# Performance work log

Hardware: AMD Instinct MI355X
Metric: run time of the kernel (lower is better)

## Reference

```python
import jax, jax.numpy as jnp
import numpy as np

N = 100000      # nodes
E = 800000      # edges (before self-loops)
G = 128         # graphs
IN = 64         # per-table embedding dim (6 tables -> 384 input features)
L = 128         # layer_embd
OUT = 128       # out_embd
H = 2           # attention heads (concat=False -> mean over heads)
VOCABS = [33, 5, 3, 4, 2, 3]
NEG_SLOPE = 0.2
BN_EPS = 1e-5


def _seg_softmax(logits, seg, n):
    # softmax of per-edge/per-node logits grouped by segment id
    m = jax.ops.segment_max(logits, seg, num_segments=n)
    e = jnp.exp(logits - m[seg])
    s = jax.ops.segment_sum(e, seg, num_segments=n)
    return e / (s[seg] + 1e-16)


def _gat_conv(x, W, a_src, a_dst, b, src, dst, n):
    # PyG GATConv, add_self_loops already applied to (src,dst), concat=False
    h = (x @ W).reshape(n, H, -1)                 # [N,H,C]
    al_s = jnp.sum(h * a_src, axis=-1)            # [N,H]
    al_d = jnp.sum(h * a_dst, axis=-1)            # [N,H]
    e = jax.nn.leaky_relu(al_s[src] + al_d[dst], NEG_SLOPE)   # [E,H]
    alpha = _seg_softmax(e, dst, n)               # softmax over each dst's in-edges
    msg = h[src] * alpha[:, :, None]              # [E,H,C]
    out = jax.ops.segment_sum(msg, dst, num_segments=n)       # [N,H,C]
    return out.mean(axis=1) + b                   # head-mean + bias


def setup_inputs() -> dict:
    key = jax.random.key(0)
    ks = jax.random.split(key, 40)
    cols = [jax.random.randint(ks[i], (N, 1), 0, VOCABS[i]) for i in range(6)]
    x = jnp.concatenate(cols, axis=1).astype(jnp.int64)
    edge_index = jax.random.randint(ks[6], (2, E), 0, N).astype(jnp.int64)
    edge_type = jax.random.randint(ks[7], (E,), 0, 4).astype(jnp.int64)
    batch = jnp.sort(jax.random.randint(ks[8], (N,), 0, G)).astype(jnp.int64)
    s = 0.05
    p = {}
    for i in range(6):
        p[f"emb{i}"] = jax.random.normal(ks[10 + i], (VOCABS[i], IN)) * s
    p["W1"] = jax.random.normal(ks[16], (6 * IN, H * L)) * s
    p["as1"] = jax.random.normal(ks[17], (H, L)) * s
    p["ad1"] = jax.random.normal(ks[18], (H, L)) * s
    p["b1"] = jnp.zeros((L,))
    p["W2"] = jax.random.normal(ks[19], (L, H * OUT)) * s
    p["as2"] = jax.random.normal(ks[20], (H, OUT)) * s
    p["ad2"] = jax.random.normal(ks[21], (H, OUT)) * s
    p["b2"] = jnp.zeros((OUT,))
    p["gw1"] = jax.random.normal(ks[22], (OUT, OUT)) * s
    p["gb1"] = jnp.zeros((OUT,))
    p["bn_g"] = jnp.ones((OUT,))
    p["bn_b"] = jnp.zeros((OUT,))
    p["bn_m"] = jnp.zeros((OUT,))
    p["bn_v"] = jnp.ones((OUT,))
    p["gw2"] = jax.random.normal(ks[23], (OUT, 1)) * s
    p["gb2"] = jnp.zeros((1,))
    p["glw"] = jax.random.normal(ks[24], (OUT, 1)) * s
    p["glb"] = jnp.zeros((1,))
    return dict(x=x, edge_index=edge_index, edge_type=edge_type, batch=batch, **p)


def reference(x, edge_index, edge_type, batch,
              emb0, emb1, emb2, emb3, emb4, emb5,
              W1, as1, ad1, b1, W2, as2, ad2, b2,
              gw1, gb1, bn_g, bn_b, bn_m, bn_v, gw2, gb2, glw, glb):
    n = x.shape[0]
    embs = [emb0, emb1, emb2, emb3, emb4, emb5]
    x_ = jnp.concatenate([embs[i][x[:, i]] for i in range(6)], axis=1)  # [N, 6*IN]
    loops = jnp.arange(n)
    src = jnp.concatenate([edge_index[0], loops])
    dst = jnp.concatenate([edge_index[1], loops])
    out = jax.nn.sigmoid(_gat_conv(x_, W1, as1, ad1, b1, src, dst, n))
    out = jax.nn.sigmoid(_gat_conv(out, W2, as2, ad2, b2, src, dst, n))
    # GlobalAttention pooling (eval-mode BatchNorm in gate_nn)
    gh = out @ gw1 + gb1
    gh = (gh - bn_m) / jnp.sqrt(bn_v + BN_EPS) * bn_g + bn_b
    gh = jax.nn.relu(gh)
    logits = gh @ gw2 + gb2                       # [N,1]
    gate = _seg_softmax(logits, batch, G)         # softmax over nodes per graph
    pooled = jax.ops.segment_sum(gate * out, batch, num_segments=G)  # [G,OUT]
    return jax.nn.sigmoid(pooled @ glw + glb)     # [G,1]
```

## Files before the change

kernel.cpp:

```cpp
#include <hip/hip_runtime.h>
#include <hip/hip_bf16.h>
#include <hip/hip_fp16.h>

#define NN 100000
#define EE 800000
#define GG 128

typedef short bf16x8 __attribute__((ext_vector_type(8)));
typedef float f32x4 __attribute__((ext_vector_type(4)));
typedef float f32x2 __attribute__((ext_vector_type(2)));

__device__ __forceinline__ float bf2f(unsigned short v) {
    union { unsigned int u; float f; } x; x.u = ((unsigned int)v) << 16; return x.f;
}
__device__ __forceinline__ unsigned short f2bf(float f) {
    union { float f; unsigned int u; } x; x.f = f;
    unsigned int r = x.u + 0x7fffu + ((x.u >> 16) & 1u);
    return (unsigned short)(r >> 16);
}
__device__ __forceinline__ float sigmoidf_(float x) { return 1.f / (1.f + __expf(-x)); }
__device__ __forceinline__ float ldp(const void* p, int i, int f) {
    return f ? ((const float*)p)[i] : bf2f(((const unsigned short*)p)[i]);
}

#if defined(__has_builtin)
#if __has_builtin(__builtin_amdgcn_cvt_pk_f32_fp8) && __has_builtin(__builtin_amdgcn_cvt_pk_fp8_f32)
#define USE_HW_FP8 1
#endif
#endif
#ifndef USE_HW_FP8
#define USE_HW_FP8 0
#endif

#if USE_HW_FP8
__device__ __forceinline__ int fp8_pack2(float a, float b) {
    return __builtin_amdgcn_cvt_pk_fp8_f32(a, b, 0, false);
}
__device__ __forceinline__ void fp8_dec4v(unsigned int q, f32x2& lo, f32x2& hi) {
    lo = __builtin_amdgcn_cvt_pk_f32_fp8((int)q, false);
    hi = __builtin_amdgcn_cvt_pk_f32_fp8((int)q, true);
}
#else
__device__ __forceinline__ unsigned char f2bf8(float f) {
    unsigned short u = __half_as_ushort(__float2half(f));
    unsigned short r = u + 0x7f + ((u >> 8) & 1);
    return (unsigned char)(r >> 8);
}
__device__ __forceinline__ int fp8_pack2(float a, float b) {
    return (int)f2bf8(a) | ((int)f2bf8(b) << 8);
}
__device__ __forceinline__ float bf8_dec(unsigned int b) {
    return __half2float(__ushort_as_half((unsigned short)(b << 8)));
}
__device__ __forceinline__ void fp8_dec4v(unsigned int q, f32x2& lo, f32x2& hi) {
    lo[0] = bf8_dec(q & 0xff); lo[1] = bf8_dec((q >> 8) & 0xff);
    hi[0] = bf8_dec((q >> 16) & 0xff); hi[1] = bf8_dec(q >> 24);
}
#endif

__global__ void k_probe2(const unsigned int* __restrict__ w, const int* __restrict__ ei,
                         int* __restrict__ fflag, int* __restrict__ iflag) {
    __shared__ int s[256];
    int t = threadIdx.x;
    if (blockIdx.x == 0) {
        int cnt = 0;
        for (int i = t; i < 1024; i += 256) {
            unsigned int v = w[i];
            int e = (v >> 7) & 0xff;
            cnt += (e >= 100 && e <= 127) ? 1 : 0;
        }
        s[t] = cnt; __syncthreads();
        for (int d = 128; d > 0; d >>= 1) { if (t < d) s[t] += s[t + d]; __syncthreads(); }
        if (t == 0) fflag[0] = (s[0] >= 512) ? 0 : 1;
    } else {
        int nz = 0;
        for (int i = t; i < 1024; i += 256) nz |= ei[2 * i + 1];
        s[t] = nz; __syncthreads();
        for (int d = 128; d > 0; d >>= 1) { if (t < d) s[t] |= s[t + d]; __syncthreads(); }
        if (t == 0) iflag[0] = (s[0] == 0) ? 1 : 0;
    }
}

__global__ void k_cvt(const int* __restrict__ xi, const int* __restrict__ ei,
                      const int* __restrict__ bi, const int* __restrict__ flag,
                      int* __restrict__ xn, int* __restrict__ srcn,
                      int* __restrict__ dstn, int* __restrict__ batchn,
                      int* __restrict__ count) {
    int j = blockIdx.x * 256 + threadIdx.x;
    int f = flag[0];
    const int XT = NN * 6, ET = 2 * EE;
    if (j < XT) xn[j] = f ? xi[2 * j] : xi[j];
    int je = j - XT;
    if (je >= 0 && je < ET) {
        int v = f ? ei[2 * je] : ei[je];
        if (je < EE) srcn[je] = v;
        else { dstn[je - EE] = v; atomicAdd(&count[v], 1); }
    }
    int jb = j - XT - ET;
    if (jb >= 0 && jb < NN) batchn[jb] = f ? bi[2 * jb] : bi[jb];
}

__global__ void k_chunk_sum(const int* __restrict__ count, int* __restrict__ csum) {
    __shared__ int s[256];
    int t = threadIdx.x;
    int base = blockIdx.x * 1024 + t * 4;
    int acc = 0;
    #pragma unroll
    for (int j = 0; j < 4; j++) { int n = base + j; if (n < NN) acc += count[n]; }
    s[t] = acc; __syncthreads();
    for (int d = 128; d > 0; d >>= 1) { if (t < d) s[t] += s[t + d]; __syncthreads(); }
    if (t == 0) csum[blockIdx.x] = s[0];
}

__global__ void k_chunk_scan(const int* __restrict__ csum, int* __restrict__ coff, int nchunk) {
    __shared__ int s[256];
    int t = threadIdx.x;
    int v = (t < nchunk) ? csum[t] : 0;
    s[t] = v; __syncthreads();
    for (int d = 1; d < 256; d <<= 1) {
        int x = (t >= d) ? s[t - d] : 0;
        __syncthreads(); s[t] += x; __syncthreads();
    }
    if (t < nchunk) coff[t] = s[t] - v;
}

__global__ void k_scan_write(const int* __restrict__ count, const int* __restrict__ coff,
                             int* __restrict__ offset, int* __restrict__ cursor) {
    __shared__ int s[256];
    int t = threadIdx.x;
    int base = blockIdx.x * 1024 + t * 4;
    int v[4]; int acc = 0;
    #pragma unroll
    for (int j = 0; j < 4; j++) { v[j] = (base + j < NN) ? count[base + j] : 0; acc += v[j]; }
    s[t] = acc; __syncthreads();
    for (int d = 1; d < 256; d <<= 1) {
        int x = (t >= d) ? s[t - d] : 0;
        __syncthreads(); s[t] += x; __syncthreads();
    }
    int pre = s[t] - acc + coff[blockIdx.x];
    #pragma unroll
    for (int j = 0; j < 4; j++) {
        if (base + j < NN) { offset[base + j] = pre; cursor[base + j] = pre; pre += v[j]; }
    }
}

__global__ void k_scatter(const int* __restrict__ src, const int* __restrict__ dst,
                          int* __restrict__ cursor, int* __restrict__ sorted) {
    int e = blockIdx.x * 256 + threadIdx.x;
    if (e < EE) {
        int d = dst[e];
        int p = atomicAdd(&cursor[d], 1);
        sorted[p] = src[e];
    }
}

__global__ void k_cvtp(const void* e0, const void* e1, const void* e2,
                       const void* e3, const void* e4, const void* e5,
                       const void* W1, const void* W2,
                       const void* as1, const void* ad1, const void* b1,
                       const void* as2, const void* ad2, const void* b2,
                       const void* gw1, const void* gb1,
                       const void* bng, const void* bnb, const void* bnm, const void* bnv,
                       const void* gw2, const void* gb2, const void* glw, const void* glb,
                       const int* __restrict__ fflag,
                       unsigned short* __restrict__ embc,
                       unsigned short* __restrict__ W1T, unsigned short* __restrict__ W2T,
                       unsigned short* __restrict__ GWT, float* __restrict__ gb1p,
                       float* __restrict__ vs1, float* __restrict__ vd1,
                       float* __restrict__ vs2, float* __restrict__ vd2,
                       float* __restrict__ vb1, float* __restrict__ vb2,
                       float* __restrict__ gw2f, float* __restrict__ glwf,
                       float* __restrict__ gb2f, float* __restrict__ glbf) {
    int i = blockIdx.x * 256 + threadIdx.x;
    int f = fflag[0];
    if (i < 98304) { int k = i / 256, n = i % 256; W1T[n * 384 + k] = f2bf(ldp(W1, i, f)); }
    if (i < 32768) { int k = i / 256, n = i % 256; W2T[n * 128 + k] = f2bf(ldp(W2, i, f)); }
    if (i < 16384) {
        int n = i >> 7, k = i & 127;
        float sc = ldp(bng, n, f) * rsqrtf(ldp(bnv, n, f) + 1e-5f);
        GWT[i] = f2bf(ldp(gw1, k * 128 + n, f) * sc);
    }
    if (i < 3200) {
        const void* src; int base;
        if (i < 2112)      { src = e0; base = 0; }
        else if (i < 2432) { src = e1; base = 2112; }
        else if (i < 2624) { src = e2; base = 2432; }
        else if (i < 2880) { src = e3; base = 2624; }
        else if (i < 3008) { src = e4; base = 2880; }
        else               { src = e5; base = 3008; }
        embc[i] = f2bf(ldp(src, i - base, f));
    }
    if (i < 256) {
        vs1[i] = ldp(as1, i, f); vd1[i] = ldp(ad1, i, f);
        vs2[i] = ldp(as2, i, f); vd2[i] = ldp(ad2, i, f);
    }
    if (i < 128) {
        vb1[i] = ldp(b1, i, f); vb2[i] = ldp(b2, i, f);
        gw2f[i] = ldp(gw2, i, f); glwf[i] = ldp(glw, i, f);
        float sc = ldp(bng, i, f) * rsqrtf(ldp(bnv, i, f) + 1e-5f);
        gb1p[i] = (ldp(gb1, i, f) - ldp(bnm, i, f)) * sc + ldp(bnb, i, f);
    }
    if (i == 0) { gb2f[0] = ldp(gb2, 0, f); glbf[0] = ldp(glb, 0, f); }
}

__global__ __launch_bounds__(256, 2) void k_gemm(
    const unsigned short* __restrict__ Ain, const int* __restrict__ xidx,
    const unsigned short* __restrict__ embc,
    const unsigned short* __restrict__ WT, unsigned char* __restrict__ H8,
    const float* __restrict__ avs, const float* __restrict__ avd,
    float* __restrict__ alS, float* __restrict__ alD,
    int K, int mode)
{
    __shared__ __align__(16) unsigned short As[64 * 32];
    __shared__ __align__(16) unsigned short Bs[256 * 32];
    const int tab_base[6] = {0, 2112, 2432, 2624, 2880, 3008};
    int tid = threadIdx.x;
    int wave = tid >> 6, lane = tid & 63;
    int quad = lane >> 4, lr = lane & 15;
    int m0 = blockIdx.x * 64;

    f32x4 zero4 = {0.f, 0.f, 0.f, 0.f};
    f32x4 acc[16];
    #pragma unroll
    for (int j = 0; j < 16; j++) acc[j] = zero4;

    for (int k0 = 0; k0 < K; k0 += 32) {
        {
            int row = tid >> 2, part = tid & 3;
            int gr = m0 + row; if (gr >= NN) gr = NN - 1;
            const unsigned short* sp;
            if (mode == 0) {
                int tbl = k0 >> 6;
                int off = k0 & 63;
                int v = xidx[gr * 6 + tbl];
                sp = embc + tab_base[tbl] + v * 64 + off + part * 8;
            } else {
                sp = Ain + (size_t)gr * K + k0 + part * 8;
            }
            int g = ((row >> 4) << 6) + (part << 4) + (row & 15);
            g ^= (part << 1);
            *(uint4*)(&As[g * 8]) = *(const uint4*)sp;
        }
        #pragma unroll
        for (int i = 0; i < 4; i++) {
            int idx = tid + i * 256;
            int row = idx >> 2, part = idx & 3;
            int g = ((row >> 4) << 6) + (part << 4) + (row & 15);
            g ^= (part << 1);
            *(uint4*)(&Bs[g * 8]) =
                *(const uint4*)(WT + (size_t)row * K + k0 + part * 8);
        }
        __syncthreads();

        int sw = (quad << 1);
        bf16x8 af0 = *(const bf16x8*)(&As[((wave * 64 + lane) ^ sw) * 8]);
        #pragma unroll
        for (int ni = 0; ni < 16; ni++) {
            bf16x8 bfv = *(const bf16x8*)(&Bs[((ni * 64 + lane) ^ sw) * 8]);
            acc[ni] = __builtin_amdgcn_mfma_f32_16x16x32_bf16(af0, bfv, acc[ni], 0, 0, 0);
        }
        __syncthreads();
    }

    float svv[16], dvv[16];
    #pragma unroll
    for (int ni = 0; ni < 16; ni++) { svv[ni] = avs[ni * 16 + lr]; dvv[ni] = avd[ni * 16 + lr]; }
    #pragma unroll
    for (int r = 0; r < 4; r++) {
        int grow = m0 + wave * 16 + quad * 4 + r;
        float ps0 = 0.f, ps1 = 0.f, pd0 = 0.f, pd1 = 0.f;
        if (grow < NN) {
            #pragma unroll
            for (int ni = 0; ni < 16; ni += 2) {
                float v0 = acc[ni][r], v1 = acc[ni + 1][r];
                int pk = fp8_pack2(v0, v1);
                H8[(size_t)grow * 256 + ni * 16 + lr] = (unsigned char)(pk & 0xff);
                H8[(size_t)grow * 256 + (ni + 1) * 16 + lr] = (unsigned char)((pk >> 8) & 0xff);
                if (ni < 8) { ps0 += v0 * svv[ni] + v1 * svv[ni + 1]; pd0 += v0 * dvv[ni] + v1 * dvv[ni + 1]; }
                else        { ps1 += v0 * svv[ni] + v1 * svv[ni + 1]; pd1 += v0 * dvv[ni] + v1 * dvv[ni + 1]; }
            }
        }
        #pragma unroll
        for (int m = 1; m < 16; m <<= 1) {
            ps0 += __shfl_xor(ps0, m); ps1 += __shfl_xor(ps1, m);
            pd0 += __shfl_xor(pd0, m); pd1 += __shfl_xor(pd1, m);
        }
        if (lr == 0 && grow < NN) {
            alS[grow * 2 + 0] = ps0; alS[grow * 2 + 1] = ps1;
            alD[grow * 2 + 0] = pd0; alD[grow * 2 + 1] = pd1;
        }
    }
}

__device__ __forceinline__ float edge_w(float e) {
    e = e > 0.f ? e : 0.2f * e;
    e = fminf(fmaxf(e, -60.f), 60.f);
    return __expf(e);
}
__global__ __launch_bounds__(256) void k_agg(const unsigned char* __restrict__ H8,
                                             const float* __restrict__ alS, const float* __restrict__ alD,
                                             const int* __restrict__ sorted, const int* __restrict__ offs,
                                             const int* __restrict__ cnts,
                                             const float* __restrict__ bias,
                                             unsigned short* __restrict__ Out) {
    __shared__ uint4 lw[4][64];
    int wid = threadIdx.x >> 6;
    int node = blockIdx.x * 4 + wid;
    if (node >= NN) return;
    int lane = threadIdx.x & 63;
    int head = lane >> 5;
    float2 adv = *(const float2*)(alD + node * 2);
    float myAd = head ? adv.y : adv.x;
    const unsigned char* Hl = H8 + lane * 4;

    float ws = edge_w(alS[node * 2 + head] + myAd);
    unsigned int qv = *(const unsigned int*)(Hl + ((unsigned)node << 8));
    f32x2 lo, hi; fp8_dec4v(qv, lo, hi);
    float den = ws;
    f32x2 wsv = {ws, ws};
    f32x2 n01 = lo * wsv, n23 = hi * wsv;

    int off = offs[node], cnt = cnts[node];
    for (int c = 0; c < cnt; c += 64) {
        int m = cnt - c; if (m > 64) m = 64;
        int j = off + c + (lane < m ? lane : 0);
        int s = sorted[j];
        float2 asv = *(const float2*)(alS + s * 2);
        float w0 = edge_w(asv.x + adv.x);
        float w1 = edge_w(asv.y + adv.y);
        lw[wid][lane] = make_uint4((unsigned)s << 8, __float_as_uint(w0), __float_as_uint(w1), 0u);
        int i = 0;
        for (; i + 8 <= m; i += 8) {
            uint4 e[8];
            #pragma unroll
            for (int u = 0; u < 8; u++) e[u] = lw[wid][i + u];
            unsigned q[8];
            #pragma unroll
            for (int u = 0; u < 8; u++) q[u] = *(const unsigned int*)(Hl + e[u].x);
            #pragma unroll
            for (int u = 0; u < 8; u++) {
                float w = __uint_as_float(head ? e[u].z : e[u].y);
                f32x2 l, h; fp8_dec4v(q[u], l, h);
                den += w;
                f32x2 wv = {w, w};
                n01 += l * wv;
                n23 += h * wv;
            }
        }
        for (; i + 4 <= m; i += 4) {
            uint4 e[4];
            #pragma unroll
            for (int u = 0; u < 4; u++) e[u] = lw[wid][i + u];
            unsigned q[4];
            #pragma unroll
            for (int u = 0; u < 4; u++) q[u] = *(const unsigned int*)(Hl + e[u].x);
            #pragma unroll
            for (int u = 0; u < 4; u++) {
                float w = __uint_as_float(head ? e[u].z : e[u].y);
                f32x2 l, h; fp8_dec4v(q[u], l, h);
                den += w;
                f32x2 wv = {w, w};
                n01 += l * wv;
                n23 += h * wv;
            }
        }
        for (; i < m; i++) {
            uint4 e0 = lw[wid][i];
            unsigned q0 = *(const unsigned int*)(Hl + e0.x);
            float w = __uint_as_float(head ? e0.z : e0.y);
            f32x2 l, h; fp8_dec4v(q0, l, h);
            den += w;
            f32x2 wv = {w, w};
            n01 += l * wv;
            n23 += h * wv;
        }
    }
    float inv = 1.f / den;
    float v0 = n01[0] * inv, v1 = n01[1] * inv, v2 = n23[0] * inv, v3 = n23[1] * inv;
    float o0 = 0.5f * (v0 + __shfl_xor(v0, 32));
    float o1 = 0.5f * (v1 + __shfl_xor(v1, 32));
    float o2 = 0.5f * (v2 + __shfl_xor(v2, 32));
    float o3 = 0.5f * (v3 + __shfl_xor(v3, 32));
    if (lane < 32) {
        int c = lane * 4;
        float4 bv = *(const float4*)(bias + c);
        o0 = sigmoidf_(o0 + bv.x);
        o1 = sigmoidf_(o1 + bv.y);
        o2 = sigmoidf_(o2 + bv.z);
        o3 = sigmoidf_(o3 + bv.w);
        uint2 pv;
        pv.x = (unsigned int)f2bf(o0) | ((unsigned int)f2bf(o1) << 16);
        pv.y = (unsigned int)f2bf(o2) | ((unsigned int)f2bf(o3) << 16);
        *(uint2*)(Out + (size_t)node * 128 + c) = pv;
    }
}

__global__ __launch_bounds__(256, 2) void k_gatemm(
    const unsigned short* __restrict__ Obuf,
    const unsigned short* __restrict__ GWT,
    const float* __restrict__ gb1p, const float* __restrict__ gw2f,
    const float* __restrict__ gb2f, float* __restrict__ logits)
{
    __shared__ __align__(16) unsigned short As[64 * 32];
    __shared__ __align__(16) unsigned short Bs[128 * 32];
    int tid = threadIdx.x;
    int wave = tid >> 6, lane = tid & 63;
    int quad = lane >> 4, lr = lane & 15;
    int m0 = blockIdx.x * 64;

    f32x4 zero4 = {0.f, 0.f, 0.f, 0.f};
    f32x4 acc[8];
    #pragma unroll
    for (int j = 0; j < 8; j++) acc[j] = zero4;

    for (int k0 = 0; k0 < 128; k0 += 32) {
        {
            int row = tid >> 2, part = tid & 3;
            int gr = m0 + row; if (gr >= NN) gr = NN - 1;
            int g = ((row >> 4) << 6) + (part << 4) + (row & 15);
            g ^= (part << 1);
            *(uint4*)(&As[g * 8]) =
                *(const uint4*)(Obuf + (size_t)gr * 128 + k0 + part * 8);
        }
        #pragma unroll
        for (int i = 0; i < 2; i++) {
            int idx = tid + i * 256;
            int row = idx >> 2, part = idx & 3;
            int g = ((row >> 4) << 6) + (part << 4) + (row & 15);
            g ^= (part << 1);
            *(uint4*)(&Bs[g * 8]) =
                *(const uint4*)(GWT + (size_t)row * 128 + k0 + part * 8);
        }
        __syncthreads();

        int sw = (quad << 1);
        bf16x8 af0 = *(const bf16x8*)(&As[((wave * 64 + lane) ^ sw) * 8]);
        #pragma unroll
        for (int ni = 0; ni < 8; ni++) {
            bf16x8 bfv = *(const bf16x8*)(&Bs[((ni * 64 + lane) ^ sw) * 8]);
            acc[ni] = __builtin_amdgcn_mfma_f32_16x16x32_bf16(af0, bfv, acc[ni], 0, 0, 0);
        }
        __syncthreads();
    }

    float gb[8], gw[8];
    #pragma unroll
    for (int ni = 0; ni < 8; ni++) { gb[ni] = gb1p[ni * 16 + lr]; gw[ni] = gw2f[ni * 16 + lr]; }
    #pragma unroll
    for (int r = 0; r < 4; r++) {
        int grow = m0 + wave * 16 + quad * 4 + r;
        float part = 0.f;
        #pragma unroll
        for (int ni = 0; ni < 8; ni++) {
            float v = acc[ni][r] + gb[ni];
            v = v > 0.f ? v : 0.f;
            part += v * gw[ni];
        }
        #pragma unroll
        for (int m = 1; m < 16; m <<= 1) part += __shfl_xor(part, m);
        if (lr == 0 && grow < NN) logits[grow] = part + gb2f[0];
    }
}

__device__ int lbound(const int* a, int n, int key) {
    int lo = 0, hi = n;
    while (lo < hi) { int mid = (lo + hi) >> 1; if (a[mid] < key) lo = mid + 1; else hi = mid; }
    return lo;
}

__global__ __launch_bounds__(256) void k_gmax(const float* __restrict__ logits,
                                              const int* __restrict__ batch,
                                              float* __restrict__ gmax) {
    __shared__ int sb[2];
    __shared__ float sm[256];
    int g = blockIdx.x, t = threadIdx.x;
    if (t < 2) sb[t] = lbound(batch, NN, g + t);
    __syncthreads();
    int lo = sb[0], hi = sb[1];
    float mx = -1e30f;
    for (int i = lo + t; i < hi; i += 256) mx = fmaxf(mx, logits[i]);
    sm[t] = mx; __syncthreads();
    for (int s = 128; s > 0; s >>= 1) { if (t < s) sm[t] = fmaxf(sm[t], sm[t + s]); __syncthreads(); }
    if (t == 0) gmax[g] = sm[0];
}

#define NPB 256
__global__ __launch_bounds__(256) void k_ppart(const unsigned short* __restrict__ Out2,
                                               const float* __restrict__ logits,
                                               const int* __restrict__ batch,
                                               const float* __restrict__ gmax,
                                               float* __restrict__ accv,
                                               float* __restrict__ accw) {
    int t = threadIdx.x;
    int c = t & 127, half = t >> 7;
    int b0 = blockIdx.x * NPB;
    int b1 = b0 + NPB; if (b1 > NN) b1 = NN;
    float acc = 0.f, aw = 0.f;
    int g = -1;
    for (int i = b0 + half; i < b1; i += 2) {
        int gi = batch[i];
        if (gi != g) {
            if (g >= 0) {
                atomicAdd(&accv[g * 128 + c], acc);
                if (c == 0) atomicAdd(&accw[g], aw);
            }
            g = gi; acc = 0.f; aw = 0.f;
        }
        float w = __expf(logits[i] - gmax[gi]);
        acc += w * bf2f(Out2[(size_t)i * 128 + c]);
        if (c == 0) aw += w;
    }
    if (g >= 0) {
        atomicAdd(&accv[g * 128 + c], acc);
        if (c == 0) atomicAdd(&accw[g], aw);
    }
}

__global__ __launch_bounds__(128) void k_pfin(const float* __restrict__ accv,
                                              const float* __restrict__ accw,
                                              const float* __restrict__ glwf,
                                              const float* __restrict__ glbf,
                                              const int* __restrict__ fflag,
                                              void* __restrict__ out) {
    __shared__ float sv[128];
    int g = blockIdx.x, t = threadIdx.x;
    float pooled = accv[g * 128 + t] / (accw[g] + 1e-16f);
    sv[t] = pooled * glwf[t];
    __syncthreads();
    for (int s = 64; s > 0; s >>= 1) { if (t < s) sv[t] += sv[t + s]; __syncthreads(); }
    if (t == 0) {
        float r = sigmoidf_(sv[0] + glbf[0]);
        if (fflag[0]) ((float*)out)[g] = r;
        else ((unsigned short*)out)[g] = f2bf(r);
    }
}

extern "C" void kernel_launch(void* const* d_in, const int* in_sizes, int n_in,
                              void* d_out, int out_size, void* d_ws, size_t ws_size,
                              hipStream_t stream) {
    const int* x_raw  = (const int*)d_in[0];
    const int* ei_raw = (const int*)d_in[1];
    const int* b_raw  = (const int*)d_in[3];

    char* p = (char*)d_ws;
    auto alloc = [&](size_t bytes) { void* r = (void*)p; p += (bytes + 255) & ~(size_t)255; return r; };
    unsigned char* H8   = (unsigned char*)alloc((size_t)NN * 256);
    unsigned short* Obuf = (unsigned short*)alloc((size_t)NN * 128 * 2);
    float* alS   = (float*)alloc((size_t)NN * 2 * 4);
    float* alD   = (float*)alloc((size_t)NN * 2 * 4);
    float* logit = (float*)alloc((size_t)NN * 4);
    char* z0 = p;
    int* count   = (int*)alloc((size_t)NN * 4);
    float* accv  = (float*)alloc(GG * 128 * 4);
    float* accw  = (float*)alloc(GG * 4);
    size_t zlen = (size_t)(p - z0);
    int* offs    = (int*)alloc((size_t)NN * 4);
    int* cursor  = (int*)alloc((size_t)NN * 4);
    int* sorted  = (int*)alloc((size_t)EE * 4);
    int* csum    = (int*)alloc(256 * 4);
    int* coff    = (int*)alloc(256 * 4);
    unsigned short* W1T  = (unsigned short*)alloc(256 * 384 * 2);
    unsigned short* W2T  = (unsigned short*)alloc(256 * 128 * 2);
    unsigned short* GWT  = (unsigned short*)alloc(128 * 128 * 2);
    float* gb1p = (float*)alloc(128 * 4);
    int* xn     = (int*)alloc((size_t)NN * 6 * 4);
    int* srcn   = (int*)alloc((size_t)EE * 4);
    int* dstn   = (int*)alloc((size_t)EE * 4);
    int* batchn = (int*)alloc((size_t)NN * 4);
    int* iflag  = (int*)alloc(256);
    int* fflag  = (int*)alloc(256);
    unsigned short* embc = (unsigned short*)alloc(3200 * 2);
    float* vs1  = (float*)alloc(256 * 4);
    float* vd1  = (float*)alloc(256 * 4);
    float* vs2  = (float*)alloc(256 * 4);
    float* vd2  = (float*)alloc(256 * 4);
    float* vb1  = (float*)alloc(128 * 4);
    float* vb2  = (float*)alloc(128 * 4);
    float* gw2f = (float*)alloc(128 * 4);
    float* glwf = (float*)alloc(128 * 4);
    float* gb2f = (float*)alloc(4);
    float* glbf = (float*)alloc(4);
    float* gmax = (float*)alloc(GG * 4);

    const int NCHUNK = (NN + 1023) / 1024;
    const int NBM = (NN + 63) / 64;
    const int NBE = (EE + 255) / 256;
    const int NB4 = (NN + 3) / 4;
    const int CVT_TOT = NN * 6 + 2 * EE + NN;

    hipMemsetAsync(z0, 0, zlen, stream);

    k_probe2<<<2, 256, 0, stream>>>((const unsigned int*)d_in[10], ei_raw, fflag, iflag);
    k_cvt<<<(CVT_TOT + 255) / 256, 256, 0, stream>>>(x_raw, ei_raw, b_raw, iflag,
                                                     xn, srcn, dstn, batchn, count);
    k_cvtp<<<(98304 + 255) / 256, 256, 0, stream>>>(
        d_in[4], d_in[5], d_in[6], d_in[7], d_in[8], d_in[9],
        d_in[10], d_in[14],
        d_in[11], d_in[12], d_in[13], d_in[15], d_in[16], d_in[17],
        d_in[18], d_in[19], d_in[20], d_in[21], d_in[22], d_in[23],
        d_in[24], d_in[25], d_in[26], d_in[27],
        fflag, embc, W1T, W2T, GWT, gb1p,
        vs1, vd1, vs2, vd2, vb1, vb2, gw2f, glwf, gb2f, glbf);

    k_chunk_sum<<<NCHUNK, 256, 0, stream>>>(count, csum);
    k_chunk_scan<<<1, 256, 0, stream>>>(csum, coff, NCHUNK);
    k_scan_write<<<NCHUNK, 256, 0, stream>>>(count, coff, offs, cursor);
    k_scatter<<<NBE, 256, 0, stream>>>(srcn, dstn, cursor, sorted);

    k_gemm<<<NBM, 256, 0, stream>>>(nullptr, xn, embc, W1T, H8, vs1, vd1, alS, alD, 384, 0);
    k_agg<<<NB4, 256, 0, stream>>>(H8, alS, alD, sorted, offs, count, vb1, Obuf);

    k_gemm<<<NBM, 256, 0, stream>>>(Obuf, xn, embc, W2T, H8, vs2, vd2, alS, alD, 128, 1);
    k_agg<<<NB4, 256, 0, stream>>>(H8, alS, alD, sorted, offs, count, vb2, Obuf);

    k_gatemm<<<NBM, 256, 0, stream>>>(Obuf, GWT, gb1p, gw2f, gb2f, logit);
    k_gmax<<<GG, 256, 0, stream>>>(logit, batchn, gmax);
    k_ppart<<<(NN + NPB - 1) / NPB, 256, 0, stream>>>(Obuf, logit, batchn, gmax, accv, accw);
    k_pfin<<<GG, 128, 0, stream>>>(accv, accw, glwf, glbf, fflag, d_out);
}
```

Measured before the change: 456.1 us.

## Precompute per-vocab embedding projections and replace first-layer GEMM with table sums

Since the first-layer input is a concatenation of six embedding lookups, x@W1 equals the sum of six per-table projections. The change precomputes a 50x256 fp32 table of each vocabulary row projected through its slice of W1, then builds each node's features by gathering and adding six rows, and also computes the attention logits and fp8 output. This replaces a K=384 MFMA GEMM over 100k nodes with a small gather-add kernel. Accumulation is now fp32 rather than bf16 inputs, so numerics differ slightly.

```diff
diff --git a/kernel.cpp b/kernel.cpp
--- a/kernel.cpp
+++ b/kernel.cpp
@@ -154,17 +154,14 @@
     }
 }
 
-__global__ void k_cvtp(const void* e0, const void* e1, const void* e2,
-                       const void* e3, const void* e4, const void* e5,
-                       const void* W1, const void* W2,
+__global__ void k_cvtp(const void* W2,
                        const void* as1, const void* ad1, const void* b1,
                        const void* as2, const void* ad2, const void* b2,
                        const void* gw1, const void* gb1,
                        const void* bng, const void* bnb, const void* bnm, const void* bnv,
                        const void* gw2, const void* gb2, const void* glw, const void* glb,
                        const int* __restrict__ fflag,
-                       unsigned short* __restrict__ embc,
-                       unsigned short* __restrict__ W1T, unsigned short* __restrict__ W2T,
+                       unsigned short* __restrict__ W2T,
                        unsigned short* __restrict__ GWT, float* __restrict__ gb1p,
                        float* __restrict__ vs1, float* __restrict__ vd1,
                        float* __restrict__ vs2, float* __restrict__ vd2,
@@ -173,23 +170,12 @@
                        float* __restrict__ gb2f, float* __restrict__ glbf) {
     int i = blockIdx.x * 256 + threadIdx.x;
     int f = fflag[0];
-    if (i < 98304) { int k = i / 256, n = i % 256; W1T[n * 384 + k] = f2bf(ldp(W1, i, f)); }
     if (i < 32768) { int k = i / 256, n = i % 256; W2T[n * 128 + k] = f2bf(ldp(W2, i, f)); }
     if (i < 16384) {
         int n = i >> 7, k = i & 127;
         float sc = ldp(bng, n, f) * rsqrtf(ldp(bnv, n, f) + 1e-5f);
         GWT[i] = f2bf(ldp(gw1, k * 128 + n, f) * sc);
     }
-    if (i < 3200) {
-        const void* src; int base;
-        if (i < 2112)      { src = e0; base = 0; }
-        else if (i < 2432) { src = e1; base = 2112; }
-        else if (i < 2624) { src = e2; base = 2432; }
-        else if (i < 2880) { src = e3; base = 2624; }
-        else if (i < 3008) { src = e4; base = 2880; }
-        else               { src = e5; base = 3008; }
-        embc[i] = f2bf(ldp(src, i - base, f));
-    }
     if (i < 256) {
         vs1[i] = ldp(as1, i, f); vd1[i] = ldp(ad1, i, f);
         vs2[i] = ldp(as2, i, f); vd2[i] = ldp(ad2, i, f);
@@ -203,17 +189,74 @@
     if (i == 0) { gb2f[0] = ldp(gb2, 0, f); glbf[0] = ldp(glb, 0, f); }
 }
 
+__constant__ int c_vbase[7] = {0, 33, 38, 41, 45, 47, 50};
+__global__ __launch_bounds__(256) void k_prep_p(
+    const void* e0, const void* e1, const void* e2,
+    const void* e3, const void* e4, const void* e5,
+    const void* W1, const int* __restrict__ fflag,
+    float* __restrict__ P) {
+    int r = blockIdx.x;
+    int c = threadIdx.x;
+    int f = fflag[0];
+    int t = 0;
+    while (r >= c_vbase[t + 1]) t++;
+    int v = r - c_vbase[t];
+    const void* emb = (t == 0) ? e0 : (t == 1) ? e1 : (t == 2) ? e2 :
+                      (t == 3) ? e3 : (t == 4) ? e4 : e5;
+    float acc = 0.f;
+    #pragma unroll 8
+    for (int k = 0; k < 64; k++) {
+        acc += ldp(emb, v * 64 + k, f) * ldp(W1, (t * 64 + k) * 256 + c, f);
+    }
+    P[r * 256 + c] = acc;
+}
+
+__global__ __launch_bounds__(256) void k_embsum(
+    const int* __restrict__ xn, const float* __restrict__ P,
+    const float* __restrict__ avs, const float* __restrict__ avd,
+    unsigned char* __restrict__ H8,
+    float* __restrict__ alS, float* __restrict__ alD) {
+    int node = blockIdx.x * 4 + (threadIdx.x >> 6);
+    if (node >= NN) return;
+    int lane = threadIdx.x & 63;
+    int c0 = lane * 4;
+    int ix[6];
+    #pragma unroll
+    for (int t = 0; t < 6; t++) ix[t] = (c_vbase[t] + xn[node * 6 + t]) * 256 + c0;
+    float4 a = *(const float4*)(P + ix[0]);
+    #pragma unroll
+    for (int t = 1; t < 6; t++) {
+        float4 b = *(const float4*)(P + ix[t]);
+        a.x += b.x; a.y += b.y; a.z += b.z; a.w += b.w;
+    }
+    float4 sv = *(const float4*)(avs + c0);
+    float4 dv = *(const float4*)(avd + c0);
+    float ps = a.x * sv.x + a.y * sv.y + a.z * sv.z + a.w * sv.w;
+    float pd = a.x * dv.x + a.y * dv.y + a.z * dv.z + a.w * dv.w;
+    #pragma unroll
+    for (int m = 1; m < 32; m <<= 1) {
+        ps += __shfl_xor(ps, m);
+        pd += __shfl_xor(pd, m);
+    }
+    if ((lane & 31) == 0) {
+        int head = lane >> 5;
+        alS[node * 2 + head] = ps;
+        alD[node * 2 + head] = pd;
+    }
+    unsigned int u = ((unsigned)fp8_pack2(a.x, a.y) & 0xffffu) |
+                     ((unsigned)fp8_pack2(a.z, a.w) << 16);
+    *(unsigned int*)(H8 + (size_t)node * 256 + c0) = u;
+}
+
 __global__ __launch_bounds__(256, 2) void k_gemm(
-    const unsigned short* __restrict__ Ain, const int* __restrict__ xidx,
-    const unsigned short* __restrict__ embc,
+    const unsigned short* __restrict__ Ain,
     const unsigned short* __restrict__ WT, unsigned char* __restrict__ H8,
     const float* __restrict__ avs, const float* __restrict__ avd,
     float* __restrict__ alS, float* __restrict__ alD,
-    int K, int mode)
+    int K)
 {
     __shared__ __align__(16) unsigned short As[64 * 32];
     __shared__ __align__(16) unsigned short Bs[256 * 32];
-    const int tab_base[6] = {0, 2112, 2432, 2624, 2880, 3008};
     int tid = threadIdx.x;
     int wave = tid >> 6, lane = tid & 63;
     int quad = lane >> 4, lr = lane & 15;
@@ -228,18 +271,9 @@
         {
             int row = tid >> 2, part = tid & 3;
             int gr = m0 + row; if (gr >= NN) gr = NN - 1;
-            const unsigned short* sp;
-            if (mode == 0) {
-                int tbl = k0 >> 6;
-                int off = k0 & 63;
-                int v = xidx[gr * 6 + tbl];
-                sp = embc + tab_base[tbl] + v * 64 + off + part * 8;
-            } else {
-                sp = Ain + (size_t)gr * K + k0 + part * 8;
-            }
             int g = ((row >> 4) << 6) + (part << 4) + (row & 15);
             g ^= (part << 1);
-            *(uint4*)(&As[g * 8]) = *(const uint4*)sp;
+            *(uint4*)(&As[g * 8]) = *(const uint4*)(Ain + (size_t)gr * K + k0 + part * 8);
         }
         #pragma unroll
         for (int i = 0; i < 4; i++) {
@@ -559,17 +593,16 @@
     int* sorted  = (int*)alloc((size_t)EE * 4);
     int* csum    = (int*)alloc(256 * 4);
     int* coff    = (int*)alloc(256 * 4);
-    unsigned short* W1T  = (unsigned short*)alloc(256 * 384 * 2);
     unsigned short* W2T  = (unsigned short*)alloc(256 * 128 * 2);
     unsigned short* GWT  = (unsigned short*)alloc(128 * 128 * 2);
     float* gb1p = (float*)alloc(128 * 4);
+    float* Ptab = (float*)alloc(50 * 256 * 4);
     int* xn     = (int*)alloc((size_t)NN * 6 * 4);
     int* srcn   = (int*)alloc((size_t)EE * 4);
     int* dstn   = (int*)alloc((size_t)EE * 4);
     int* batchn = (int*)alloc((size_t)NN * 4);
     int* iflag  = (int*)alloc(256);
     int* fflag  = (int*)alloc(256);
-    unsigned short* embc = (unsigned short*)alloc(3200 * 2);
     float* vs1  = (float*)alloc(256 * 4);
     float* vd1  = (float*)alloc(256 * 4);
     float* vs2  = (float*)alloc(256 * 4);
@@ -593,24 +626,25 @@
     k_probe2<<<2, 256, 0, stream>>>((const unsigned int*)d_in[10], ei_raw, fflag, iflag);
     k_cvt<<<(CVT_TOT + 255) / 256, 256, 0, stream>>>(x_raw, ei_raw, b_raw, iflag,
                                                      xn, srcn, dstn, batchn, count);
-    k_cvtp<<<(98304 + 255) / 256, 256, 0, stream>>>(
-        d_in[4], d_in[5], d_in[6], d_in[7], d_in[8], d_in[9],
-        d_in[10], d_in[14],
+    k_cvtp<<<(32768 + 255) / 256, 256, 0, stream>>>(
+        d_in[14],
         d_in[11], d_in[12], d_in[13], d_in[15], d_in[16], d_in[17],
         d_in[18], d_in[19], d_in[20], d_in[21], d_in[22], d_in[23],
         d_in[24], d_in[25], d_in[26], d_in[27],
-        fflag, embc, W1T, W2T, GWT, gb1p,
+        fflag, W2T, GWT, gb1p,
         vs1, vd1, vs2, vd2, vb1, vb2, gw2f, glwf, gb2f, glbf);
+    k_prep_p<<<50, 256, 0, stream>>>(d_in[4], d_in[5], d_in[6], d_in[7], d_in[8], d_in[9],
+                                     d_in[10], fflag, Ptab);
 
     k_chunk_sum<<<NCHUNK, 256, 0, stream>>>(count, csum);
     k_chunk_scan<<<1, 256, 0, stream>>>(csum, coff, NCHUNK);
     k_scan_write<<<NCHUNK, 256, 0, stream>>>(count, coff, offs, cursor);
     k_scatter<<<NBE, 256, 0, stream>>>(srcn, dstn, cursor, sorted);
 
-    k_gemm<<<NBM, 256, 0, stream>>>(nullptr, xn, embc, W1T, H8, vs1, vd1, alS, alD, 384, 0);
+    k_embsum<<<NB4, 256, 0, stream>>>(xn, Ptab, vs1, vd1, H8, alS, alD);
     k_agg<<<NB4, 256, 0, stream>>>(H8, alS, alD, sorted, offs, count, vb1, Obuf);
 
-    k_gemm<<<NBM, 256, 0, stream>>>(Obuf, xn, embc, W2T, H8, vs2, vd2, alS, alD, 128, 1);
+    k_gemm<<<NBM, 256, 0, stream>>>(Obuf, W2T, H8, vs2, vd2, alS, alD, 128);
     k_agg<<<NB4, 256, 0, stream>>>(H8, alS, alD, sorted, offs, count, vb2, Obuf);
 
     k_gatemm<<<NBM, 256, 0, stream>>>(Obuf, GWT, gb1p, gw2f, gb2f, logit);
```

Measured after the change: 458.1 us. About the same (+0.4%).
